# Kernel tuning notes

Hardware: AMD Instinct MI355X
Metric: run time of the kernel (lower is better)

The kernel has to match this reference:

```python
import jax, jax.numpy as jnp
import numpy as np

TRIANGLE_TABLE = np.array([
    [-1,-1,-1,-1,-1,-1],[1,0,2,-1,-1,-1],[4,0,3,-1,-1,-1],[1,4,2,1,3,4],
    [3,1,5,-1,-1,-1],[2,3,0,2,5,3],[1,4,0,1,5,4],[4,2,5,-1,-1,-1],
    [4,5,2,-1,-1,-1],[4,1,0,4,5,1],[3,2,0,3,5,2],[1,3,5,-1,-1,-1],
    [4,1,2,4,3,1],[3,0,4,-1,-1,-1],[2,0,1,-1,-1,-1],[-1,-1,-1,-1,-1,-1]], dtype=np.int32)
NUM_TRI_TABLE = np.array([0,1,1,2,1,2,2,1,1,2,2,1,2,1,1,0], dtype=np.int32)
BASE_TET_EDGES = np.array([0,1,0,2,0,3,1,2,1,3,2,3], dtype=np.int32)

NV = 200_000
NT = 800_000

def setup_inputs() -> dict:
    key = jax.random.key(0)
    k1, k2, k3 = jax.random.split(key, 3)
    pos_nx3 = jax.random.normal(k1, (NV, 3), dtype=jnp.float32)
    sdf_n = jax.random.normal(k2, (NV,), dtype=jnp.float32)
    tet_fx4 = jax.random.randint(k3, (NT, 4), 0, NV, dtype=jnp.int32)
    return {"pos_nx3": pos_nx3, "sdf_n": sdf_n, "tet_fx4": tet_fx4}

def map_uv(face_gidx, max_idx):
    # Faithful port of DMTet.map_uv: one 2-triangle UV quad per (potential) tet.
    N = int(np.ceil(np.sqrt((max_idx + 1) // 2)))
    lin = jnp.linspace(0.0, 1.0 - 1.0 / N, N, dtype=jnp.float32)
    tex_y, tex_x = jnp.meshgrid(lin, lin, indexing='ij')
    pad = 0.9 / N
    uvs = jnp.stack([tex_x, tex_y, tex_x + pad, tex_y,
                     tex_x + pad, tex_y + pad, tex_x, tex_y + pad], axis=-1).reshape(-1, 2)
    t = face_gidx // 2
    tet_idx = (t // N) * N + (t % N)   # identity for t < N*N, kept faithful
    tri_idx = face_gidx % 2
    uv_idx = jnp.stack([tet_idx * 4, tet_idx * 4 + tri_idx + 1, tet_idx * 4 + tri_idx + 2], axis=-1)
    return uvs, uv_idx.reshape(-1, 3)

def reference(pos_nx3, sdf_n, tet_fx4):
    # NOTE: marching-tets output sizes are data dependent -> eager (non-jit) jax,
    # matching the torch.unique / boolean-mask structure of the original.
    tri_table = jnp.asarray(TRIANGLE_TABLE)
    num_tri_table = jnp.asarray(NUM_TRI_TABLE)
    base_edges = jnp.asarray(BASE_TET_EDGES)

    occ_n = sdf_n > 0                                   # [Nv]
    occ_fx4 = occ_n[tet_fx4]                            # [T,4]
    occ_sum = occ_fx4.sum(-1)
    valid_tets = (occ_sum > 0) & (occ_sum < 4)

    tet_valid = tet_fx4[valid_tets]                     # [Tv,4]
    all_edges = tet_valid[:, base_edges].reshape(-1, 2) # [Tv*6,2]
    all_edges = jnp.sort(all_edges, axis=1)             # == sort_edges
    unique_edges, idx_map = jnp.unique(all_edges, axis=0, return_inverse=True)

    mask_edges = occ_n[unique_edges].sum(-1) == 1       # sign-crossing edges
    mapping = jnp.where(mask_edges, jnp.cumsum(mask_edges) - 1, -1)
    idx_map = mapping[idx_map.reshape(-1)].reshape(-1, 6)
    interp_v = unique_edges[mask_edges]                 # [Ne,2]

    # linear interpolation of crossing point along each edge
    p = pos_nx3[interp_v]                               # [Ne,2,3]
    s = sdf_n[interp_v] * jnp.array([1.0, -1.0], dtype=sdf_n.dtype)  # negate 2nd sdf
    denom = s.sum(1, keepdims=True)                     # [Ne,1]
    w = s[:, ::-1] / denom                              # flip + normalize
    verts = (p * w[:, :, None]).sum(1)                  # [Ne,3]

    v_id = jnp.array([1, 2, 4, 8], dtype=jnp.int32)
    tetindex = (occ_fx4[valid_tets].astype(jnp.int32) * v_id).sum(-1)  # [Tv]
    num_triangles = num_tri_table[tetindex]
    m1 = num_triangles == 1
    m2 = num_triangles == 2
    f1 = jnp.take_along_axis(idx_map[m1], tri_table[tetindex[m1]][:, :3], axis=1).reshape(-1, 3)
    f2 = jnp.take_along_axis(idx_map[m2], tri_table[tetindex[m2]][:, :6], axis=1).reshape(-1, 3)
    faces = jnp.concatenate([f1, f2], axis=0)

    num_tets = tet_fx4.shape[0]
    tet_gidx = jnp.arange(num_tets, dtype=jnp.int32)[valid_tets]
    face_gidx = jnp.concatenate([
        tet_gidx[m1] * 2,
        jnp.stack([tet_gidx[m2] * 2, tet_gidx[m2] * 2 + 1], axis=-1).reshape(-1)], axis=0)

    uvs, uv_idx = map_uv(face_gidx, num_tets * 2)
    return verts, faces, uvs, uv_idx
```

## Files before the change

### kernel.cpp

```cpp
#include <hip/hip_runtime.h>
#include <cstdio>
#include <cstdint>

typedef unsigned long long u64;

static const int kNV = 200000;
static const int kNT = 800000;
static const int kNUV = 895;
#define UVS_ROWS   3204100LL
#define UVS_FLOATS 6408200LL
#define CAP 3300000

#define NH 392
#define TILE_T 2048
#define BINW 64
#define BSH 6
#define NBIN 3125
#define SUBSH 15
#define FINEB 512
#define MAXBIN 2816

__device__ const int c_tri[16][6] = {
    {-1,-1,-1,-1,-1,-1},{1,0,2,-1,-1,-1},{4,0,3,-1,-1,-1},{1,4,2,1,3,4},
    {3,1,5,-1,-1,-1},{2,3,0,2,5,3},{1,4,0,1,5,4},{4,2,5,-1,-1,-1},
    {4,5,2,-1,-1,-1},{4,1,0,4,5,1},{3,2,0,3,5,2},{1,3,5,-1,-1,-1},
    {4,1,2,4,3,1},{3,0,4,-1,-1,-1},{2,0,1,-1,-1,-1},{-1,-1,-1,-1,-1,-1}};
__device__ const int c_ntri[16]   = {0,1,1,2,1,2,2,1,1,2,2,1,2,1,1,0};
__device__ const int c_ncross[16] = {0,3,3,4,3,4,4,3,3,4,4,3,4,3,3,0};
__device__ const int c_edges[12] = {0,1,0,2,0,3,1,2,1,3,2,3};

#define PK(m1,m2,nc) (((u64)(m1) << 44) | ((u64)(m2) << 24) | (u64)(nc))

#define SCAN_B 256
#define SCAN_I 8
#define SCAN_TILE (SCAN_B*SCAN_I)

template<typename T>
__global__ void k_scan_partial(const T* __restrict__ in, T* __restrict__ partials, int n){
  __shared__ T sm[SCAN_B];
  int b = blockIdx.x;
  long long base = (long long)b*SCAN_TILE;
  T sum = 0;
  for (int i = threadIdx.x; i < SCAN_TILE; i += SCAN_B){
    long long idx = base + i;
    if (idx < n) sum += in[idx];
  }
  sm[threadIdx.x] = sum; __syncthreads();
  for (int s = SCAN_B/2; s > 0; s >>= 1){
    if ((int)threadIdx.x < s) sm[threadIdx.x] += sm[threadIdx.x + s];
    __syncthreads();
  }
  if (threadIdx.x == 0) partials[b] = sm[0];
}

template<typename T>
__global__ void k_scan_blocksums(T* __restrict__ partials, int nb, T* __restrict__ total_out){
  __shared__ T sm[SCAN_B];
  T carry = 0;
  for (int base = 0; base < nb; base += SCAN_B){
    int i = base + (int)threadIdx.x;
    T v = (i < nb) ? partials[i] : (T)0;
    sm[threadIdx.x] = v; __syncthreads();
    for (int off = 1; off < SCAN_B; off <<= 1){
      T t = ((int)threadIdx.x >= off) ? sm[threadIdx.x - off] : (T)0;
      __syncthreads();
      sm[threadIdx.x] += t;
      __syncthreads();
    }
    if (i < nb) partials[i] = carry + sm[threadIdx.x] - v;
    T tilesum = sm[SCAN_B-1];
    __syncthreads();
    carry += tilesum;
  }
  if (threadIdx.x == 0 && total_out) *total_out = carry;
}

template<typename T>
__global__ void k_scan_apply(const T* __restrict__ in, T* __restrict__ out,
                             const T* __restrict__ partials, int n){
  __shared__ T sm[SCAN_B];
  int b = blockIdx.x;
  long long base = (long long)b*SCAN_TILE + (long long)threadIdx.x*SCAN_I;
  T v[SCAN_I]; T s = 0;
  #pragma unroll
  for (int k = 0; k < SCAN_I; k++){ long long idx = base + k; v[k] = (idx < n) ? in[idx] : (T)0; s += v[k]; }
  sm[threadIdx.x] = s; __syncthreads();
  for (int off = 1; off < 256; off <<= 1){
    T t = ((int)threadIdx.x >= off) ? sm[threadIdx.x - off] : (T)0;
    __syncthreads();
    sm[threadIdx.x] += t;
    __syncthreads();
  }
  T excl = sm[threadIdx.x] - s + partials[b];
  #pragma unroll
  for (int k = 0; k < SCAN_I; k++){ long long idx = base + k; if (idx < n) out[idx] = excl; excl += v[k]; }
}

template<typename T>
static void run_scan(const T* in, T* out, int n, T* partials, hipStream_t s){
  int nb = (n + SCAN_TILE - 1) / SCAN_TILE;
  k_scan_partial<T><<<nb, SCAN_B, 0, s>>>(in, partials, n);
  k_scan_blocksums<T><<<1, SCAN_B, 0, s>>>(partials, nb, out + n);
  k_scan_apply<T><<<nb, SCAN_B, 0, s>>>(in, out, partials, n);
}


__global__ void k_classify_hist(const int* __restrict__ tet, const float* __restrict__ sdf,
                                int* __restrict__ tetinfo, u64* __restrict__ pk,
                                int* __restrict__ blockHist, u64* __restrict__ pkPart){
  __shared__ int h[NBIN];
  __shared__ u64 red[256];
  int blk = blockIdx.x;
  for (int j = threadIdx.x; j < NBIN; j += 256) h[j] = 0;
  __syncthreads();
  int t0 = blk*TILE_T;
  u64 myPk = 0;
  for (int k = 0; k < TILE_T/256; k++){
    int t = t0 + k*256 + threadIdx.x;
    if (t < kNT){
      int4 v4 = ((const int4*)tet)[t];
      int pat = ((sdf[v4.x] > 0.0f) ? 1 : 0) | ((sdf[v4.y] > 0.0f) ? 2 : 0)
              | ((sdf[v4.z] > 0.0f) ? 4 : 0) | ((sdf[v4.w] > 0.0f) ? 8 : 0);
      tetinfo[t] = pat;
      int nt_ = c_ntri[pat];
      u64 pv = PK(nt_ == 1, nt_ == 2, c_ncross[pat]);
      pk[t] = pv;
      myPk += pv;
      if (pat != 0 && pat != 15){
        int vv[4] = {v4.x, v4.y, v4.z, v4.w};
        #pragma unroll
        for (int e = 0; e < 6; e++){
          int i0 = c_edges[2*e], i1 = c_edges[2*e+1];
          if (((pat >> i0) & 1) != ((pat >> i1) & 1)){
            int a = vv[i0], b = vv[i1]; if (a > b){ int tm = a; a = b; b = tm; }
            atomicAdd(&h[a >> BSH], 1);
          }
        }
      }
    }
  }
  red[threadIdx.x] = myPk;
  __syncthreads();
  for (int s = 128; s > 0; s >>= 1){
    if ((int)threadIdx.x < s) red[threadIdx.x] += red[threadIdx.x + s];
    __syncthreads();
  }
  if (threadIdx.x == 0) pkPart[blk] = red[0];
  for (int j = threadIdx.x; j < NBIN; j += 256) blockHist[j*NH + blk] = h[j];
}

__global__ void k_scatter(const int* __restrict__ tet, const int* __restrict__ tetinfo,
                          const u64* __restrict__ psum, const int* __restrict__ bhScan,
                          u64* __restrict__ ebin){
  __shared__ int c[NBIN];
  int blk = blockIdx.x;
  for (int j = threadIdx.x; j < NBIN; j += 256) c[j] = bhScan[j*NH + blk];
  __syncthreads();
  int t0 = blk*TILE_T;
  for (int k = 0; k < TILE_T/256; k++){
    int t = t0 + k*256 + threadIdx.x;
    if (t < kNT){
      int pat = tetinfo[t];
      if (pat != 0 && pat != 15){
        int4 v4 = ((const int4*)tet)[t];
        int vv[4] = {v4.x, v4.y, v4.z, v4.w};
        int seq = (int)(psum[t] & 0xFFFFFF);
        #pragma unroll
        for (int e = 0; e < 6; e++){
          int i0 = c_edges[2*e], i1 = c_edges[2*e+1];
          if (((pat >> i0) & 1) != ((pat >> i1) & 1)){
            int a = vv[i0], b = vv[i1]; if (a > b){ int tm = a; a = b; b = tm; }
            int pos = atomicAdd(&c[a >> BSH], 1);
            ebin[pos] = ((u64)(unsigned)a << 40) | ((u64)(unsigned)b << 22) | (unsigned)seq;
            seq++;
          }
        }
      }
    }
  }
}

__global__ void k_fineflags(const int* __restrict__ bhScan, const u64* __restrict__ ebin,
                            u64* __restrict__ efin, unsigned* __restrict__ meta,
                            int* __restrict__ binFirstCnt){
  __shared__ u64 ld[MAXBIN];
  __shared__ unsigned char fl[MAXBIN];
  __shared__ int fp[MAXBIN];
  __shared__ int h[FINEB];
  __shared__ int ss[256];
  int bin = blockIdx.x, tid = threadIdx.x;
  int binStart = bhScan[bin*NH];
  int binEnd   = bhScan[(bin+1)*NH];
  int n = binEnd - binStart;
  int a0 = bin << BSH;
  for (int j = tid; j < FINEB; j += 256) h[j] = 0;
  __syncthreads();
  if (n <= MAXBIN){
    for (int i = tid; i < n; i += 256){
      u64 p = ebin[binStart + i];
      int key = (((int)(p >> 40) - a0) << 3) | ((int)((p >> 22) & 0x3FFFF) >> SUBSH);
      atomicAdd(&h[key], 1);
    }
    __syncthreads();
    int s0 = h[2*tid], s1 = h[2*tid+1];
    int pair = s0 + s1;
    ss[tid] = pair; __syncthreads();
    for (int off = 1; off < 256; off <<= 1){
      int v = (tid >= off) ? ss[tid-off] : 0;
      __syncthreads(); ss[tid] += v; __syncthreads();
    }
    int excl = ss[tid] - pair;
    h[2*tid] = excl; h[2*tid+1] = excl + s0;
    __syncthreads();
    for (int i = tid; i < n; i += 256){
      u64 p = ebin[binStart + i];
      int key = (((int)(p >> 40) - a0) << 3) | ((int)((p >> 22) & 0x3FFFF) >> SUBSH);
      ld[atomicAdd(&h[key], 1)] = p;
    }
    __syncthreads();
    for (int x = tid; x < n; x += 256){
      u64 key = ld[x] >> 22; u64 grp = key >> SUBSH;
      unsigned char f = 1;
      for (int y = x-1; y >= 0; y--){
        u64 ky = ld[y] >> 22;
        if ((ky >> SUBSH) != grp) break;
        if (ky == key){ f = 0; break; }
      }
      fl[x] = f;
    }
    __syncthreads();
    const int C = MAXBIN/256;
    int cbase = tid*C;
    int loc[C]; int cs = 0;
    #pragma unroll
    for (int q = 0; q < C; q++){ int idx = cbase+q; loc[q] = (idx < n) ? fl[idx] : 0; cs += loc[q]; }
    ss[tid] = cs; __syncthreads();
    for (int off = 1; off < 256; off <<= 1){
      int v = (tid >= off) ? ss[tid-off] : 0;
      __syncthreads(); ss[tid] += v; __syncthreads();
    }
    int ex2 = ss[tid] - cs;
    #pragma unroll
    for (int q = 0; q < C; q++){ fp[cbase+q] = ex2; ex2 += loc[q]; }
    __syncthreads();
    for (int x = tid; x < n; x += 256){
      u64 p = ld[x];
      u64 key = p >> 22; u64 grp = key >> SUBSH;
      int sx = x; while (sx > 0 && ((ld[sx-1] >> 22) >> SUBSH) == grp) sx--;
      int ex = x+1; while (ex < n && ((ld[ex] >> 22) >> SUBSH) == grp) ex++;
      int rk = 0;
      for (int y = sx; y < ex; y++){ if (fl[y] && (ld[y] >> 22) < key) rk++; }
      int rp = fp[sx] + rk;
      efin[binStart + x] = p;
      meta[binStart + x] = ((unsigned)bin << 13) | ((unsigned)rp << 1) | (unsigned)fl[x];
    }
    if (tid == 255) binFirstCnt[bin] = ss[255];
  } else {
    for (int i = binStart + tid; i < binEnd; i += 256){
      u64 p = ebin[i];
      int key = (((int)(p >> 40) - a0) << 3) | ((int)((p >> 22) & 0x3FFFF) >> SUBSH);
      atomicAdd(&h[key], 1);
    }
    __syncthreads();
    int s0 = h[2*tid], s1 = h[2*tid+1];
    int pair = s0 + s1;
    ss[tid] = pair; __syncthreads();
    for (int off = 1; off < 256; off <<= 1){
      int v = (tid >= off) ? ss[tid-off] : 0;
      __syncthreads(); ss[tid] += v; __syncthreads();
    }
    int excl = ss[tid] - pair;
    h[2*tid] = excl; h[2*tid+1] = excl + s0;
    __syncthreads();
    for (int i = binStart + tid; i < binEnd; i += 256){
      u64 p = ebin[i];
      int key = (((int)(p >> 40) - a0) << 3) | ((int)((p >> 22) & 0x3FFFF) >> SUBSH);
      efin[binStart + atomicAdd(&h[key], 1)] = p;
    }
    __syncthreads();
    if (tid == 0){
      int fcnt = 0;
      for (int x = 0; x < n; x++){
        u64 key = efin[binStart+x] >> 22; u64 grp = key >> SUBSH;
        int sx = x; while (sx > 0 && ((efin[binStart+sx-1] >> 22) >> SUBSH) == grp) sx--;
        int f = 1;
        for (int y = sx; y < x; y++) if ((efin[binStart+y] >> 22) == key){ f = 0; break; }
        int fb = 0;
        for (int y = 0; y < sx; y++){
          u64 ky = efin[binStart+y] >> 22; u64 gy = ky >> SUBSH;
          int sy = y; while (sy > 0 && ((efin[binStart+sy-1] >> 22) >> SUBSH) == gy) sy--;
          int fy = 1;
          for (int z = sy; z < y; z++) if ((efin[binStart+z] >> 22) == ky){ fy = 0; break; }
          fb += fy;
        }
        int ex = x+1; while (ex < n && ((efin[binStart+ex] >> 22) >> SUBSH) == grp) ex++;
        int rk = 0;
        for (int y = sx; y < ex; y++){
          u64 ky = efin[binStart+y] >> 22;
          if (ky < key){
            int fy = 1;
            for (int z = sx; z < y; z++) if ((efin[binStart+z] >> 22) == ky){ fy = 0; break; }
            if (fy) rk++;
          }
        }
        if (f) fcnt++;
        meta[binStart+x] = ((unsigned)bin << 13) | ((unsigned)(fb+rk) << 1) | (unsigned)f;
      }
      binFirstCnt[bin] = fcnt;
    }
  }
}

__global__ void k_emit(const u64* __restrict__ efin, const int* __restrict__ totp,
                       const int* __restrict__ binPref, const unsigned* __restrict__ meta,
                       const float* __restrict__ pos, const float* __restrict__ sdf,
                       float* __restrict__ out, int* __restrict__ rankBySeq){
  int total = *totp;
  int i = blockIdx.x*256 + threadIdx.x;
  if (i >= total) return;
  u64 p = efin[i];
  unsigned m = meta[i];
  int first = m & 1;
  int rp = (m >> 1) & 0xFFF;
  int bin = m >> 13;
  int r = binPref[bin] + rp;
  rankBySeq[(int)(p & 0x3FFFFF)] = r;
  if (first){
    int a = (int)(p >> 40);
    int b = (int)((p >> 22) & 0x3FFFF);
    float sa = sdf[a], sb = sdf[b];
    float denom = sa - sb;
    float w0 = (-sb) / denom;
    float w1 = sa / denom;
    out[3LL*r + 0] = pos[3*a+0]*w0 + pos[3*b+0]*w1;
    out[3LL*r + 1] = pos[3*a+1]*w0 + pos[3*b+1]*w1;
    out[3LL*r + 2] = pos[3*a+2]*w0 + pos[3*b+2]*w1;
  }
}

__global__ void k_faces(const int* __restrict__ tetinfo, const u64* __restrict__ psum,
                        const int* __restrict__ Nep, const int* __restrict__ rankBySeq,
                        float* __restrict__ out){
  int t = blockIdx.x*256 + threadIdx.x; if (t >= kNT) return;
  int pat = tetinfo[t];
  int nt_ = c_ntri[pat];
  if (nt_ == 0) return;
  u64 tot = psum[kNT];
  int Nm1 = (int)(tot >> 44), Nm2 = (int)((tot >> 24) & 0xFFFFF);
  int Ne = *Nep;
  long long faces_off = 3LL*Ne;
  long long uvidx_off = faces_off + 3LL*((long long)Nm1 + 2LL*Nm2) + UVS_FLOATS;
  u64 ps = psum[t];
  int m1v = (int)(ps >> 44), m2v = (int)((ps >> 24) & 0xFFFFF);
  int seq = (int)(ps & 0xFFFFFF);
  int er[6];
  int j = 0;
  #pragma unroll
  for (int e = 0; e < 6; e++){
    int i0 = c_edges[2*e], i1 = c_edges[2*e+1];
    if (((pat >> i0) & 1) != ((pat >> i1) & 1)){
      er[e] = rankBySeq[seq + j];
      j++;
    } else er[e] = -1;
  }
  for (int k = 0; k < nt_; k++){
    long long row = (nt_ == 1) ? (long long)m1v : ((long long)Nm1 + 2LL*m2v + k);
    #pragma unroll
    for (int c = 0; c < 3; c++){
      int slot = c_tri[pat][3*k + c];
      out[faces_off + 3*row + c] = (float)er[slot];
    }
    out[uvidx_off + 3*row + 0] = (float)(4*t);
    out[uvidx_off + 3*row + 1] = (float)(4*t + k + 1);
    out[uvidx_off + 3*row + 2] = (float)(4*t + k + 2);
  }
}

__global__ void k_uvs(const u64* __restrict__ psum, const int* __restrict__ Nep,
                      float* __restrict__ out){
  long long r = (long long)blockIdx.x*256 + threadIdx.x;
  if (r >= UVS_ROWS) return;
  u64 tot = psum[kNT];
  int Nm1 = (int)(tot >> 44), Nm2 = (int)((tot >> 24) & 0xFFFFF);
  int Ne = *Nep;
  long long off = 3LL*Ne + 3LL*((long long)Nm1 + 2LL*Nm2);
  int cell = (int)(r >> 2), k = (int)(r & 3);
  int iy = cell / kNUV, ix = cell - iy*kNUV;
  const float delta = (1.0f - 1.0f/895.0f) / 894.0f;
  const float pad = 0.9f / 895.0f;
  float x = (float)ix * delta, y = (float)iy * delta;
  float u = x + ((k == 1 || k == 2) ? pad : 0.0f);
  float v = y + ((k >= 2) ? pad : 0.0f);
  if ((off & 1) == 0){
    float2 uv = make_float2(u, v);
    *reinterpret_cast<float2*>(&out[off + 2*r]) = uv;
  } else {
    out[off + 2*r]     = u;
    out[off + 2*r + 1] = v;
  }
}

static inline int divup(int a, int b){ return (a + b - 1) / b; }

extern "C" void kernel_launch(void* const* d_in, const int* in_sizes, int n_in,
                              void* d_out, int out_size, void* d_ws, size_t ws_size,
                              hipStream_t stream){
  const float* pos = (const float*)d_in[0];
  const float* sdf = (const float*)d_in[1];
  const int*   tet = (const int*)d_in[2];
  float* out = (float*)d_out;

  char* ws = (char*)d_ws;
  size_t off = 0;
  auto alloc = [&](size_t bytes) -> char* {
    char* p = ws + off; off += (bytes + 255) & ~(size_t)255; return p;
  };
  int* tetinfo     = (int*)alloc((size_t)kNT*4);
  u64* pk          = (u64*)alloc((size_t)kNT*8);
  u64* psum        = (u64*)alloc((size_t)(kNT+1)*8);
  int* blockHist   = (int*)alloc((size_t)NBIN*NH*4);
  int* bhScan      = (int*)alloc((size_t)(NBIN*NH+1)*4);
  u64* ebin        = (u64*)alloc((size_t)CAP*8);
  u64* efin        = (u64*)alloc((size_t)CAP*8);
  unsigned* meta   = (unsigned*)alloc((size_t)CAP*4);
  int* rankBySeq   = (int*)alloc((size_t)CAP*4);
  int* binFirstCnt = (int*)alloc((size_t)(NBIN+1)*4);
  u64* pkPart      = (u64*)alloc((size_t)NH*8);
  int* partI       = (int*)alloc(4096*4);
  if (off > ws_size){
    fprintf(stderr, "[dmtet] workspace too small: need %zu have %zu\n", off, ws_size);
    return;
  }

  k_classify_hist<<<NH, 256, 0, stream>>>(tet, sdf, tetinfo, pk, blockHist, pkPart);
  k_scan_blocksums<u64><<<1, SCAN_B, 0, stream>>>(pkPart, NH, psum + kNT);
  k_scan_apply<u64><<<divup(kNT,SCAN_TILE), SCAN_B, 0, stream>>>(pk, psum, pkPart, kNT);
  run_scan<int>(blockHist, bhScan, NBIN*NH, partI, stream);
  k_scatter<<<NH, 256, 0, stream>>>(tet, tetinfo, psum, bhScan, ebin);
  k_fineflags<<<NBIN, 256, 0, stream>>>(bhScan, ebin, efin, meta, binFirstCnt);
  k_scan_blocksums<int><<<1, SCAN_B, 0, stream>>>(binFirstCnt, NBIN, binFirstCnt + NBIN);
  k_emit<<<divup(CAP,256), 256, 0, stream>>>(efin, bhScan + NBIN*NH, binFirstCnt, meta,
                                             pos, sdf, out, rankBySeq);
  k_faces<<<divup(kNT,256), 256, 0, stream>>>(tetinfo, psum, binFirstCnt + NBIN, rankBySeq, out);
  k_uvs<<<divup((int)UVS_ROWS,256), 256, 0, stream>>>(psum, binFirstCnt + NBIN, out);
}
```

Measured before the change: 226.2 us.

## Speed up fine-bin dedup kernel with wavefront scans and register-cached edges

Replaces the shared-memory Hillis-Steele block scans, which need many __syncthreads, with a wavefront shuffle scan plus a four-entry cross-wave sum. Edge keys are loaded once into registers and reused for both the histogram and the scatter passes instead of being re-read from global memory. Duplicate detection and rank computation now use the group boundaries left in the histogram offsets, so the linear walks to find each group's start and end are gone. It also narrows fp to unsigned short to cut LDS use, at the cost of more register pressure from the per-thread C-sized arrays.

```diff
diff --git a/kernel.cpp b/kernel.cpp
--- a/kernel.cpp
+++ b/kernel.cpp
@@ -19,6 +19,7 @@
 #define SUBSH 15
 #define FINEB 512
 #define MAXBIN 2816
+#define C 11
 
 __device__ const int c_tri[16][6] = {
     {-1,-1,-1,-1,-1,-1},{1,0,2,-1,-1,-1},{4,0,3,-1,-1,-1},{1,4,2,1,3,4},
@@ -30,6 +31,24 @@
 __device__ const int c_edges[12] = {0,1,0,2,0,3,1,2,1,3,2,3};
 
 #define PK(m1,m2,nc) (((u64)(m1) << 44) | ((u64)(m2) << 24) | (u64)(nc))
+
+__device__ __forceinline__ int blockScanExcl(int v, volatile int* wsum, int tid, int* totalOut){
+  int lane = tid & 63, wv = tid >> 6;
+  int x = v;
+  #pragma unroll
+  for (int off = 1; off < 64; off <<= 1){
+    int t = __shfl_up(x, off, 64);
+    if (lane >= off) x += t;
+  }
+  __syncthreads();
+  if (lane == 63) wsum[wv] = x;
+  __syncthreads();
+  int carry = 0;
+  #pragma unroll
+  for (int w = 0; w < 4; w++) if (w < wv) carry += wsum[w];
+  if (totalOut) *totalOut = wsum[0] + wsum[1] + wsum[2] + wsum[3];
+  return carry + x - v;
+}
 
 #define SCAN_B 256
 #define SCAN_I 8
@@ -185,9 +204,9 @@
                             int* __restrict__ binFirstCnt){
   __shared__ u64 ld[MAXBIN];
   __shared__ unsigned char fl[MAXBIN];
-  __shared__ int fp[MAXBIN];
+  __shared__ unsigned short fp[MAXBIN];
   __shared__ int h[FINEB];
-  __shared__ int ss[256];
+  __shared__ int wsum[4];
   int bin = blockIdx.x, tid = threadIdx.x;
   int binStart = bhScan[bin*NH];
   int binEnd   = bhScan[(bin+1)*NH];
@@ -196,65 +215,66 @@
   for (int j = tid; j < FINEB; j += 256) h[j] = 0;
   __syncthreads();
   if (n <= MAXBIN){
-    for (int i = tid; i < n; i += 256){
-      u64 p = ebin[binStart + i];
-      int key = (((int)(p >> 40) - a0) << 3) | ((int)((p >> 22) & 0x3FFFF) >> SUBSH);
-      atomicAdd(&h[key], 1);
-    }
+    u64 pr[C]; int kr[C];
+    #pragma unroll
+    for (int k = 0; k < C; k++){
+      int i = tid + k*256;
+      if (i < n){
+        u64 p = ebin[binStart + i];
+        pr[k] = p;
+        kr[k] = (((int)(p >> 40) - a0) << 3) | ((int)((p >> 22) & 0x3FFFF) >> SUBSH);
+      } else kr[k] = -1;
+    }
+    #pragma unroll
+    for (int k = 0; k < C; k++) if (kr[k] >= 0) atomicAdd(&h[kr[k]], 1);
     __syncthreads();
     int s0 = h[2*tid], s1 = h[2*tid+1];
-    int pair = s0 + s1;
-    ss[tid] = pair; __syncthreads();
-    for (int off = 1; off < 256; off <<= 1){
-      int v = (tid >= off) ? ss[tid-off] : 0;
-      __syncthreads(); ss[tid] += v; __syncthreads();
-    }
-    int excl = ss[tid] - pair;
+    int excl = blockScanExcl(s0 + s1, wsum, tid, nullptr);
     h[2*tid] = excl; h[2*tid+1] = excl + s0;
     __syncthreads();
-    for (int i = tid; i < n; i += 256){
-      u64 p = ebin[binStart + i];
-      int key = (((int)(p >> 40) - a0) << 3) | ((int)((p >> 22) & 0x3FFFF) >> SUBSH);
-      ld[atomicAdd(&h[key], 1)] = p;
-    }
-    __syncthreads();
-    for (int x = tid; x < n; x += 256){
-      u64 key = ld[x] >> 22; u64 grp = key >> SUBSH;
-      unsigned char f = 1;
-      for (int y = x-1; y >= 0; y--){
-        u64 ky = ld[y] >> 22;
-        if ((ky >> SUBSH) != grp) break;
-        if (ky == key){ f = 0; break; }
-      }
-      fl[x] = f;
-    }
-    __syncthreads();
-    const int C = MAXBIN/256;
+    #pragma unroll
+    for (int k = 0; k < C; k++)
+      if (kr[k] >= 0) ld[atomicAdd(&h[kr[k]], 1)] = pr[k];
+    __syncthreads();
+    #pragma unroll
+    for (int k = 0; k < C; k++){
+      int x = tid + k*256;
+      if (x < n){
+        u64 my = ld[x] >> 22;
+        int key = (((int)(my >> 18) - a0) << 3) | ((int)(my & 0x3FFFF) >> SUBSH);
+        int gs = key ? h[key-1] : 0;
+        unsigned char f = 1;
+        for (int y = x-1; y >= gs; y--){ if ((ld[y] >> 22) == my){ f = 0; break; } }
+        fl[x] = f;
+      } else if (x < MAXBIN) fl[x] = 0;
+    }
+    __syncthreads();
     int cbase = tid*C;
     int loc[C]; int cs = 0;
     #pragma unroll
-    for (int q = 0; q < C; q++){ int idx = cbase+q; loc[q] = (idx < n) ? fl[idx] : 0; cs += loc[q]; }
-    ss[tid] = cs; __syncthreads();
-    for (int off = 1; off < 256; off <<= 1){
-      int v = (tid >= off) ? ss[tid-off] : 0;
-      __syncthreads(); ss[tid] += v; __syncthreads();
-    }
-    int ex2 = ss[tid] - cs;
-    #pragma unroll
-    for (int q = 0; q < C; q++){ fp[cbase+q] = ex2; ex2 += loc[q]; }
-    __syncthreads();
-    for (int x = tid; x < n; x += 256){
-      u64 p = ld[x];
-      u64 key = p >> 22; u64 grp = key >> SUBSH;
-      int sx = x; while (sx > 0 && ((ld[sx-1] >> 22) >> SUBSH) == grp) sx--;
-      int ex = x+1; while (ex < n && ((ld[ex] >> 22) >> SUBSH) == grp) ex++;
-      int rk = 0;
-      for (int y = sx; y < ex; y++){ if (fl[y] && (ld[y] >> 22) < key) rk++; }
-      int rp = fp[sx] + rk;
-      efin[binStart + x] = p;
-      meta[binStart + x] = ((unsigned)bin << 13) | ((unsigned)rp << 1) | (unsigned)fl[x];
-    }
-    if (tid == 255) binFirstCnt[bin] = ss[255];
+    for (int q = 0; q < C; q++){ loc[q] = fl[cbase+q]; cs += loc[q]; }
+    int tot;
+    int ex2 = blockScanExcl(cs, wsum, tid, &tot);
+    #pragma unroll
+    for (int q = 0; q < C; q++){ fp[cbase+q] = (unsigned short)ex2; ex2 += loc[q]; }
+    if (tid == 0) binFirstCnt[bin] = tot;
+    __syncthreads();
+    #pragma unroll
+    for (int k = 0; k < C; k++){
+      int x = tid + k*256;
+      if (x < n){
+        u64 p = ld[x];
+        u64 my = p >> 22;
+        int key = (((int)(my >> 18) - a0) << 3) | ((int)(my & 0x3FFFF) >> SUBSH);
+        int gs = key ? h[key-1] : 0;
+        int ge = h[key];
+        int rk = 0;
+        for (int y = gs; y < ge; y++){ if (fl[y] && (ld[y] >> 22) < my) rk++; }
+        int rp = (int)fp[gs] + rk;
+        efin[binStart + x] = p;
+        meta[binStart + x] = ((unsigned)bin << 13) | ((unsigned)rp << 1) | (unsigned)fl[x];
+      }
+    }
   } else {
     for (int i = binStart + tid; i < binEnd; i += 256){
       u64 p = ebin[i];
@@ -263,13 +283,7 @@
     }
     __syncthreads();
     int s0 = h[2*tid], s1 = h[2*tid+1];
-    int pair = s0 + s1;
-    ss[tid] = pair; __syncthreads();
-    for (int off = 1; off < 256; off <<= 1){
-      int v = (tid >= off) ? ss[tid-off] : 0;
-      __syncthreads(); ss[tid] += v; __syncthreads();
-    }
-    int excl = ss[tid] - pair;
+    int excl = blockScanExcl(s0 + s1, wsum, tid, nullptr);
     h[2*tid] = excl; h[2*tid+1] = excl + s0;
     __syncthreads();
     for (int i = binStart + tid; i < binEnd; i += 256){
```

Measured after the change: 211.1 us. -6.7%, faster.
